# Kernel optimization log

Measured on AMD Instinct MI355X. Metric: run time of the kernel, lower is better.

The kernel has to match this reference:

```python
import jax, jax.numpy as jnp
import numpy as np

EPS = 1e-5
HEADS = 24
HEAD_DIM = 128


def _layernorm_noaffine(x):
    # LayerNorm over last dim (head_dim), elementwise_affine=False
    mu = jnp.mean(x, axis=-1, keepdims=True)
    var = jnp.mean(jnp.square(x - mu), axis=-1, keepdims=True)
    return (x - mu) / jnp.sqrt(var + EPS)


def _apply_rope(x, cos, sin):
    # diffusers apply_rotary_emb, use_real_unbind_dim=-2, sequence_dim=1
    # x: [B, S_img, H, D]; cos/sin: [S_img, D]
    x_real, x_imag = jnp.split(x, 2, axis=-1)               # halves of D
    x_rot = jnp.concatenate([-x_imag, x_real], axis=-1)
    return x * cos[None, :, None, :] + x_rot * sin[None, :, None, :]


def setup_inputs() -> dict:
    key = jax.random.key(0)
    ks = jax.random.split(key, 8)
    B, T, I, D = 2, 256, 1024, 3072
    inner = HEADS * HEAD_DIM
    return {
        "hidden_states": jax.random.normal(ks[0], (B, I, D), jnp.float32),
        "encoder_hidden_states": jax.random.normal(ks[1], (B, T, D), jnp.float32),
        "cos": jax.random.uniform(ks[2], (I, HEAD_DIM), jnp.float32),
        "sin": jax.random.uniform(ks[3], (I, HEAD_DIM), jnp.float32),
        "w_qkv": jax.random.normal(ks[4], (D, 3 * inner), jnp.float32) * 0.02,
        "b_qkv": jax.random.normal(ks[5], (3 * inner,), jnp.float32) * 0.02,
        "w_out": jax.random.normal(ks[6], (inner, D), jnp.float32) * 0.02,
        "b_out": jax.random.normal(ks[7], (D,), jnp.float32) * 0.02,
    }


def reference(hidden_states, encoder_hidden_states, cos, sin, w_qkv, b_qkv, w_out, b_out):
    text_len = encoder_hidden_states.shape[1]
    x = jnp.concatenate([encoder_hidden_states, hidden_states], axis=1)  # [B, S, D]
    B, S, _ = x.shape
    qkv = x @ w_qkv + b_qkv                                  # [B, S, 3*inner]
    q, k, v = jnp.split(qkv, 3, axis=-1)
    q = q.reshape(B, S, HEADS, HEAD_DIM)
    k = k.reshape(B, S, HEADS, HEAD_DIM)
    v = v.reshape(B, S, HEADS, HEAD_DIM)
    q = _layernorm_noaffine(q)
    k = _layernorm_noaffine(k)
    # partial RoPE: image tokens only
    q = jnp.concatenate([q[:, :text_len], _apply_rope(q[:, text_len:], cos, sin)], axis=1)
    k = jnp.concatenate([k[:, :text_len], _apply_rope(k[:, text_len:], cos, sin)], axis=1)
    # non-causal attention, scale = 1/sqrt(head_dim)
    scale = 1.0 / np.sqrt(HEAD_DIM).astype(np.float32)
    scores = jnp.einsum('bqhd,bkhd->bhqk', q, k) * scale
    attn = jax.nn.softmax(scores, axis=-1)
    out = jnp.einsum('bhqk,bkhd->bqhd', attn, v).reshape(B, S, HEADS * HEAD_DIM)
    out = out @ w_out + b_out                                # [B, S, D]
    return out[:, text_len:, :], out[:, :text_len, :]
```

## Files before the change

kernel.cpp:

```cpp
#include <hip/hip_runtime.h>

typedef unsigned short u16;
typedef __attribute__((ext_vector_type(8))) short bf16x8;
typedef __attribute__((ext_vector_type(4))) float f32x4;
typedef __attribute__((ext_vector_type(16))) float f32x16;

typedef const __attribute__((address_space(1))) void* gptr_t;
typedef __attribute__((address_space(3))) void* lptr_t;

__device__ __forceinline__ unsigned cvtpk_bf16(float a, float b){
  unsigned r; asm("v_cvt_pk_bf16_f32 %0, %1, %2" : "=v"(r) : "v"(a), "v"(b)); return r;
}
__device__ __forceinline__ u16 f2bf(float x){ return (u16)cvtpk_bf16(x, x); }
__device__ __forceinline__ float bf2f(u16 u){ union{unsigned i; float f;} v; v.i = ((unsigned)u)<<16; return v.f; }
__device__ __forceinline__ float fexp2(float x){ float r; asm("v_exp_f32 %0, %1" : "=v"(r) : "v"(x)); return r; }

__global__ __launch_bounds__(256) void prep_x_kernel(const float* __restrict__ hs,
                                                     const float* __restrict__ ehs,
                                                     u16* __restrict__ A){
  int idx = blockIdx.x*256 + threadIdx.x;
  int v = idx*4;
  int m = v/3072, c = v - m*3072;
  int b = m/1280, s = m - b*1280;
  const float* src = (s < 256) ? (ehs + ((size_t)(b*256+s))*3072 + c)
                               : (hs  + ((size_t)(b*1024+(s-256)))*3072 + c);
  float4 f = *(const float4*)src;
  uint2 o; o.x = cvtpk_bf16(f.x, f.y); o.y = cvtpk_bf16(f.z, f.w);
  *(uint2*)(A + v) = o;
}

__global__ __launch_bounds__(256) void transpose_w_kernel(const float* __restrict__ W,
                                                          u16* __restrict__ Wt,
                                                          int K, int N){
  __shared__ float t[64][36];
  int k0 = blockIdx.y*64, n0 = blockIdx.x*32;
  int tid = threadIdx.x;
  #pragma unroll
  for (int i=0;i<2;i++){
    int cell = i*256 + tid; int kl = cell>>3, nc = cell&7;
    *(float4*)&t[kl][nc*4] = *(const float4*)&W[(size_t)(k0+kl)*N + n0 + nc*4];
  }
  __syncthreads();
  #pragma unroll
  for (int i=0;i<2;i++){
    int chunk = i*256 + tid; int nl = chunk>>4, kc = chunk&15;
    float a = t[kc*4+0][nl], b2 = t[kc*4+1][nl], c2 = t[kc*4+2][nl], d2 = t[kc*4+3][nl];
    uint2 u; u.x = cvtpk_bf16(a, b2); u.y = cvtpk_bf16(c2, d2);
    *(uint2*)&Wt[(size_t)(n0+nl)*K + k0 + kc*4] = u;
  }
}

__global__ __launch_bounds__(512) void gemm256_kernel(const u16* __restrict__ A,
                                                      const u16* __restrict__ Bt,
                                                      const float* __restrict__ bias,
                                                      u16* __restrict__ C){
  const int K = 3072, N = 9216;
  __shared__ __align__(16) u16 lds[2][2][2][8192];
  int tid = threadIdx.x, wv = tid>>6, lane = tid&63;
  int wm = wv>>2, wn = wv&3;
  int l15 = lane&15, l4 = lane>>4;

  int bid = blockIdx.x;
  int wg = (bid&7)*45 + (bid>>3);
  int bm = wg/36, bn = wg%36;
  int m0 = bm*256, n0 = bn*256;

  int srow = tid>>2;
  int schn = (tid&3) ^ ((tid>>3)&3);
  const u16* aSrc = A  + (size_t)(m0 + srow)*K + schn*8;
  const u16* bSrc = Bt + (size_t)(n0 + srow)*K + schn*8;
  u16* ldsF = &lds[0][0][0][0];

  auto stagePair = [&](int Gp){
    int s = (Gp>>1)&1, h = Gp&1;
    size_t ko = (size_t)Gp*32;
    u16* la = ldsF + s*32768 + h*8192 + wv*512;
    u16* lb = la + 16384;
    const u16* a0 = aSrc + ko;
    const u16* b0 = bSrc + ko;
    __builtin_amdgcn_global_load_lds((gptr_t)a0,                 (lptr_t)la,        16,0,0);
    __builtin_amdgcn_global_load_lds((gptr_t)(a0+(size_t)128*K), (lptr_t)(la+4096), 16,0,0);
    __builtin_amdgcn_global_load_lds((gptr_t)b0,                 (lptr_t)lb,        16,0,0);
    __builtin_amdgcn_global_load_lds((gptr_t)(b0+(size_t)128*K), (lptr_t)(lb+4096), 16,0,0);
  };

  int fcs = l4 ^ ((l15>>1)&3);
  int aoff = (wm*128 + l15)*32 + fcs*8;
  int boff = (wn*64  + l15)*32 + fcs*8;

  f32x4 acc[8][4];
  #pragma unroll
  for (int r=0;r<8;r++)
    #pragma unroll
    for (int c=0;c<4;c++)
      #pragma unroll
      for (int q=0;q<4;q++) acc[r][c][q] = 0.f;

  stagePair(0); stagePair(1); stagePair(2);
  asm volatile("s_waitcnt vmcnt(8)" ::: "memory");
  __builtin_amdgcn_s_barrier();

  auto group = [&](int G, bool issue){
    const u16* rA = ldsF + ((G>>1)&1)*32768 + (G&1)*8192;
    const u16* rB = rA + 16384;
    bf16x8 af[8], bfv[4];
    #pragma unroll
    for (int r=0;r<8;r++) af[r] = *(const bf16x8*)(rA + aoff + r*512);
    #pragma unroll
    for (int c=0;c<4;c++) bfv[c] = *(const bf16x8*)(rB + boff + c*512);
    if (issue) stagePair(G+3);
    __builtin_amdgcn_s_setprio(1);
    #pragma unroll
    for (int r=0;r<8;r++)
      #pragma unroll
      for (int c=0;c<4;c++)
        acc[r][c] = __builtin_amdgcn_mfma_f32_16x16x32_bf16(af[r], bfv[c], acc[r][c], 0,0,0);
    __builtin_amdgcn_s_setprio(0);
  };

  for (int G=0; G<93; ++G){
    group(G, true);
    asm volatile("s_waitcnt vmcnt(8)" ::: "memory");
    __builtin_amdgcn_s_barrier();
  }
  group(93,false); asm volatile("s_waitcnt vmcnt(4)" ::: "memory"); __builtin_amdgcn_s_barrier();
  group(94,false); asm volatile("s_waitcnt vmcnt(0)" ::: "memory"); __builtin_amdgcn_s_barrier();
  group(95,false);

  #pragma unroll
  for (int r=0;r<8;r++){
    int row = m0 + wm*128 + r*16 + l4*4;
    #pragma unroll
    for (int c=0;c<4;c++){
      int col = n0 + wn*64 + c*16 + l15;
      float bv = bias[col];
      #pragma unroll
      for (int q=0;q<4;q++)
        C[(size_t)(row+q)*N + col] = f2bf(acc[r][c][q] + bv);
    }
  }
}

__global__ __launch_bounds__(256) void gemm_bt_kernel(const u16* __restrict__ A,
                                                      const u16* __restrict__ Bt,
                                                      const float* __restrict__ bias,
                                                      float* __restrict__ Cf,
                                                      int K, int N){
  __shared__ u16 As[2][4096];
  __shared__ u16 Bs[2][4096];
  int tid = threadIdx.x, wv = tid>>6, lane = tid&63;
  int l15 = lane & 15, l4 = lane >> 4;
  int m0 = blockIdx.y*128, n0 = blockIdx.x*128;
  int wr = wv>>1, wc = wv&1;

  f32x4 acc[4][4];
  #pragma unroll
  for (int i=0;i<4;i++)
    #pragma unroll
    for (int j=0;j<4;j++)
      #pragma unroll
      for (int r=0;r<4;r++) acc[i][j][r] = 0.f;

  const int NT = K >> 5;

  auto stage = [&](int buf, int kt){
    #pragma unroll
    for (int i=0;i<2;i++){
      int c = (wv*2+i)*64 + lane; int row = c>>2, kc = c&3;
      const u16* s = A + (size_t)(m0+row)*K + kt + kc*8;
      __builtin_amdgcn_global_load_lds((gptr_t)s, (lptr_t)(&As[buf][(wv*2+i)*512]), 16, 0, 0);
    }
    #pragma unroll
    for (int i=0;i<2;i++){
      int c = (wv*2+i)*64 + lane; int row = c>>2, kc = c&3;
      const u16* s = Bt + (size_t)(n0+row)*K + kt + kc*8;
      __builtin_amdgcn_global_load_lds((gptr_t)s, (lptr_t)(&Bs[buf][(wv*2+i)*512]), 16, 0, 0);
    }
  };

  stage(0, 0);
  __syncthreads();
  for (int t=0; t<NT; t++){
    int cur = t & 1;
    if (t+1 < NT) stage(cur^1, (t+1)*32);
    bf16x8 af[4], bfr[4];
    #pragma unroll
    for (int i=0;i<4;i++){
      af[i]  = *(const bf16x8*)&As[cur][(wr*64 + i*16 + l15)*32 + l4*8];
      bfr[i] = *(const bf16x8*)&Bs[cur][(wc*64 + i*16 + l15)*32 + l4*8];
    }
    #pragma unroll
    for (int i=0;i<4;i++)
      #pragma unroll
      for (int j=0;j<4;j++)
        acc[i][j] = __builtin_amdgcn_mfma_f32_16x16x32_bf16(af[i], bfr[j], acc[i][j], 0,0,0);
    __syncthreads();
  }

  #pragma unroll
  for (int i=0;i<4;i++){
    int row = m0 + wr*64 + i*16 + l4*4;
    #pragma unroll
    for (int j=0;j<4;j++){
      int col = n0 + wc*64 + j*16 + l15;
      float bv = bias[col];
      #pragma unroll
      for (int r=0;r<4;r++){
        int rr = row + r;
        int bb = rr / 1280; int s = rr - bb*1280;
        float* dst = (s < 256) ? (Cf + 6291456 + ((size_t)(bb*256 + s))*3072)
                               : (Cf + ((size_t)(bb*1024 + (s-256)))*3072);
        dst[col] = acc[i][j][r] + bv;
      }
    }
  }
}

__device__ __forceinline__ void ln_head(const u16* __restrict__ in, u16* __restrict__ out,
                                        const float* __restrict__ cosb, const float* __restrict__ sinb,
                                        int lane, int s, float scale){
  float x0 = bf2f(in[lane]), x1 = bf2f(in[64+lane]);
  float sum = x0 + x1;
  #pragma unroll
  for (int off=32; off>=1; off>>=1) sum += __shfl_xor(sum, off);
  float mean = sum * 0.0078125f;
  float d0 = x0-mean, d1 = x1-mean;
  float vs = d0*d0 + d1*d1;
  #pragma unroll
  for (int off=32; off>=1; off>>=1) vs += __shfl_xor(vs, off);
  float rstd = rsqrtf(vs*0.0078125f + 1e-5f);
  float y0 = d0*rstd, y1 = d1*rstd;
  if (s >= 256){
    int p = s - 256;
    float c0 = cosb[p*128 + lane], c1 = cosb[p*128 + 64 + lane];
    float s0 = sinb[p*128 + lane], s1 = sinb[p*128 + 64 + lane];
    float t0 = y0*c0 - y1*s0;
    float t1 = y1*c1 + y0*s1;
    y0 = t0; y1 = t1;
  }
  out[lane]    = f2bf(y0*scale);
  out[64+lane] = f2bf(y1*scale);
}

__global__ __launch_bounds__(256) void ln_rope_kernel(const u16* __restrict__ qkv,
                                                      const float* __restrict__ cosb,
                                                      const float* __restrict__ sinb,
                                                      u16* __restrict__ Q, u16* __restrict__ Kd){
  int g = blockIdx.x*4 + (threadIdx.x>>6);
  int lane = threadIdx.x & 63;
  int h = g % 24; int m = g / 24;
  int b = m / 1280; int s = m - b*1280;
  const u16* base = qkv + (size_t)m*9216 + h*128;
  size_t ho = ((size_t)(b*24 + h)*1280 + s)*128;
  ln_head(base,        Q  + ho, cosb, sinb, lane, s, 0.12751512f);
  ln_head(base + 3072, Kd + ho, cosb, sinb, lane, s, 1.0f);
}

__global__ __launch_bounds__(256) void v_transpose_kernel(const u16* __restrict__ qkv,
                                                          u16* __restrict__ Vt){
  __shared__ u16 tl[16384];
  int tid = threadIdx.x;
  int blk = blockIdx.x;
  int st = blk % 10; int bh = blk / 10; int b = bh/24, h = bh - b*24;
  #pragma unroll
  for (int i=0;i<8;i++){
    int idx = i*256 + tid; int s = idx>>4, dc = idx&15;
    int m = b*1280 + st*128 + s;
    bf16x8 v = *(const bf16x8*)(qkv + (size_t)m*9216 + 6144 + h*128 + dc*8);
    *(bf16x8*)(tl + (s*16 + (dc ^ ((s>>3)&7)))*8) = v;
  }
  __syncthreads();
  #pragma unroll
  for (int i=0;i<8;i++){
    int idx = i*256 + tid; int d = idx>>4, sc = idx&15;
    union { u16 t[8]; bf16x8 v; } tmp;
    #pragma unroll
    for (int j=0;j<8;j++){
      int s = sc*8 + j;
      tmp.t[j] = tl[(s*16 + ((d>>3) ^ ((s>>3)&7)))*8 + (d&7)];
    }
    *(bf16x8*)(Vt + ((size_t)bh*128 + d)*1280 + st*128 + sc*8) = tmp.v;
  }
}

__global__ __launch_bounds__(256) void attn_kernel(const u16* __restrict__ Q,
                                                   const u16* __restrict__ Kg,
                                                   const u16* __restrict__ Vt,
                                                   u16* __restrict__ AO){
  __shared__ __align__(16) u16 smem[32768];
  int tid = threadIdx.x, wv = tid>>6, lane = tid&63;
  int l31 = lane & 31, hi = lane >> 5;
  int blk = blockIdx.x;
  int qt = blk % 10; int bh = blk / 10;
  int b = bh / 24; int h = bh - b*24;
  const u16* Qb = Q  + (size_t)bh*1280*128;
  const u16* Kb = Kg + (size_t)bh*1280*128;
  const u16* Vb = Vt + (size_t)bh*128*1280;
  int q0 = qt*128 + wv*32;

  bf16x8 qf[8];
  #pragma unroll
  for (int ds=0; ds<8; ds++)
    qf[ds] = *(const bf16x8*)(Qb + (size_t)(q0 + l31)*128 + ds*16 + hi*8);

  f32x16 o[4];
  #pragma unroll
  for (int dc=0; dc<4; dc++)
    #pragma unroll
    for (int r=0;r<16;r++) o[dc][r] = 0.f;
  float mrun = -1e30f, lrun = 0.f;

  auto stage = [&](int t){
    int s0 = t*64; int bu = t&1;
    u16* Ksb = smem + bu*8192;
    u16* Vsb = smem + 16384 + bu*8192;
    #pragma unroll
    for (int i=0;i<4;i++){
      int c = (wv*4+i)*64 + lane; int key = c>>4, dc16 = c&15;
      const u16* src = Kb + (size_t)(s0+key)*128 + ((dc16 ^ (key&7))<<3);
      __builtin_amdgcn_global_load_lds((gptr_t)src, (lptr_t)(Ksb + (wv*4+i)*512), 16, 0, 0);
    }
    #pragma unroll
    for (int i=0;i<4;i++){
      int c = (wv*4+i)*64 + lane; int d = c>>3, kc = c&7;
      const u16* src = Vb + (size_t)d*1280 + s0 + ((kc ^ (d&7))<<3);
      __builtin_amdgcn_global_load_lds((gptr_t)src, (lptr_t)(Vsb + (wv*4+i)*512), 16, 0, 0);
    }
  };

  auto compute = [&](int t){
    const u16* Ks = smem + (t&1)*8192;
    const u16* Vs = smem + 16384 + (t&1)*8192;
    f32x16 sacc0, sacc1;
    #pragma unroll
    for (int r=0;r<16;r++){ sacc0[r]=0.f; sacc1[r]=0.f; }
    __builtin_amdgcn_s_setprio(1);
    #pragma unroll
    for (int ds=0; ds<8; ds++){
      int ch = ds*2 + hi;
      bf16x8 k0 = *(const bf16x8*)(Ks + (l31*16      + (ch ^ (l31 & 7)))*8);
      bf16x8 k1 = *(const bf16x8*)(Ks + ((32+l31)*16 + (ch ^ (l31 & 7)))*8);
      sacc0 = __builtin_amdgcn_mfma_f32_32x32x16_bf16(k0, qf[ds], sacc0, 0,0,0);
      sacc1 = __builtin_amdgcn_mfma_f32_32x32x16_bf16(k1, qf[ds], sacc1, 0,0,0);
    }
    __builtin_amdgcn_s_setprio(0);
    float mt = sacc0[0];
    #pragma unroll
    for (int r=1;r<16;r++) mt = fmaxf(mt, sacc0[r]);
    #pragma unroll
    for (int r=0;r<16;r++) mt = fmaxf(mt, sacc1[r]);
    mt = fmaxf(mt, __shfl_xor(mt, 32));
    float mnew = fmaxf(mrun, mt);
    float corr = fexp2(mrun - mnew);
    mrun = mnew;
    float p[32]; float ps = 0.f;
    #pragma unroll
    for (int r=0;r<16;r++){ p[r]    = fexp2(sacc0[r] - mnew); ps += p[r]; }
    #pragma unroll
    for (int r=0;r<16;r++){ p[16+r] = fexp2(sacc1[r] - mnew); ps += p[16+r]; }
    ps += __shfl_xor(ps, 32);
    lrun = lrun*corr + ps;
    #pragma unroll
    for (int dc=0; dc<4; dc++)
      #pragma unroll
      for (int r=0;r<16;r++) o[dc][r] *= corr;

    bf16x8 pf[4];
    #pragma unroll
    for (int c=0;c<4;c++){
      const float* pp = p + (c>>1)*16 + (c&1)*8;
      unsigned x0 = cvtpk_bf16(pp[0], pp[1]);
      unsigned y0 = cvtpk_bf16(pp[4], pp[5]);
      unsigned x1 = cvtpk_bf16(pp[2], pp[3]);
      unsigned y1 = cvtpk_bf16(pp[6], pp[7]);
      asm volatile("v_permlane32_swap_b32 %0, %1" : "+v"(x0), "+v"(y0));
      asm volatile("v_permlane32_swap_b32 %0, %1" : "+v"(x1), "+v"(y1));
      union { unsigned u[4]; bf16x8 v; } wb;
      wb.u[0]=x0; wb.u[1]=x1; wb.u[2]=y0; wb.u[3]=y1;
      pf[c] = wb.v;
    }
    __builtin_amdgcn_s_setprio(1);
    #pragma unroll
    for (int c=0;c<4;c++){
      #pragma unroll
      for (int dc=0;dc<4;dc++){
        int d = dc*32 + l31;
        bf16x8 vf = *(const bf16x8*)(Vs + (d*8 + ((2*c+hi) ^ (d&7)))*8);
        o[dc] = __builtin_amdgcn_mfma_f32_32x32x16_bf16(vf, pf[c], o[dc], 0,0,0);
      }
    }
    __builtin_amdgcn_s_setprio(0);
  };

  stage(0); stage(1);
  for (int t=0; t<19; ++t){
    asm volatile("s_waitcnt vmcnt(8)" ::: "memory");
    __builtin_amdgcn_s_barrier();
    compute(t);
    __builtin_amdgcn_s_barrier();
    if (t <= 17) stage(t+2);
  }
  asm volatile("s_waitcnt vmcnt(0)" ::: "memory");
  __builtin_amdgcn_s_barrier();
  compute(19);

  float rl = 1.f / lrun;
  __syncthreads();
  u16* ob = smem + wv*4096;
  #pragma unroll
  for (int dc=0; dc<4; dc++){
    #pragma unroll
    for (int rp=0; rp<8; rp++){
      int d = dc*32 + 2*(rp&1) + 8*(rp>>1) + 4*hi;
      unsigned u = cvtpk_bf16(o[dc][2*rp]*rl, o[dc][2*rp+1]*rl);
      int chs = (d>>3) ^ (l31 & 7);
      *(unsigned*)(ob + l31*128 + chs*8 + (d&7)) = u;
    }
  }
  __syncthreads();
  #pragma unroll
  for (int i=0;i<8;i++){
    int idx = i*64 + lane; int q = idx>>4, c8 = idx&15;
    bf16x8 vv = *(const bf16x8*)(ob + q*128 + ((c8 ^ (q&7))<<3));
    *(bf16x8*)(AO + (size_t)(b*1280 + q0 + q)*3072 + h*128 + c8*8) = vv;
  }
}

extern "C" void kernel_launch(void* const* d_in, const int* in_sizes, int n_in,
                              void* d_out, int out_size, void* d_ws, size_t ws_size,
                              hipStream_t stream){
  (void)in_sizes; (void)n_in; (void)out_size; (void)ws_size;
  const float* hs   = (const float*)d_in[0];
  const float* ehs  = (const float*)d_in[1];
  const float* cosb = (const float*)d_in[2];
  const float* sinb = (const float*)d_in[3];
  const float* wqkv = (const float*)d_in[4];
  const float* bqkv = (const float*)d_in[5];
  const float* wout = (const float*)d_in[6];
  const float* bout = (const float*)d_in[7];
  char* w = (char*)d_ws;
  size_t o = 0;
  u16* Abf = (u16*)(w + o); o += 15728640ull;
  u16* WqT = (u16*)(w + o); o += 56623104ull;
  u16* WoT = (u16*)(w + o); o += 18874368ull;
  u16* qkv = (u16*)(w + o); o += 47185920ull;
  u16* Qd  = (u16*)(w + o); o += 15728640ull;
  u16* Kd  = (u16*)(w + o); o += 15728640ull;
  u16* Vtd = (u16*)(w + o); o += 15728640ull;
  u16* AO  = (u16*)(w + o);
  float* out = (float*)d_out;

  prep_x_kernel<<<7680, 256, 0, stream>>>(hs, ehs, Abf);
  transpose_w_kernel<<<dim3(288,48), 256, 0, stream>>>(wqkv, WqT, 3072, 9216);
  transpose_w_kernel<<<dim3(96,48),  256, 0, stream>>>(wout, WoT, 3072, 3072);
  gemm256_kernel<<<360, 512, 0, stream>>>(Abf, WqT, bqkv, qkv);
  ln_rope_kernel<<<15360, 256, 0, stream>>>(qkv, cosb, sinb, Qd, Kd);
  v_transpose_kernel<<<480, 256, 0, stream>>>(qkv, Vtd);
  attn_kernel<<<480, 256, 0, stream>>>(Qd, Kd, Vtd, AO);
  gemm_bt_kernel<<<dim3(24,20), 256, 0, stream>>>(AO, WoT, bout, out, 3072, 3072);
}
```

Before: 572.0 us.

## Retile QKV GEMM to 256x192 with 4-stage LDS and add lazy softmax rescaling

```diff
diff --git a/kernel.cpp b/kernel.cpp
--- a/kernel.cpp
+++ b/kernel.cpp
@@ -14,6 +14,12 @@
 __device__ __forceinline__ u16 f2bf(float x){ return (u16)cvtpk_bf16(x, x); }
 __device__ __forceinline__ float bf2f(u16 u){ union{unsigned i; float f;} v; v.i = ((unsigned)u)<<16; return v.f; }
 __device__ __forceinline__ float fexp2(float x){ float r; asm("v_exp_f32 %0, %1" : "=v"(r) : "v"(x)); return r; }
+__device__ __forceinline__ float vmax16(f32x16 v){
+  float a0 = fmaxf(v[0],v[1]),  a1 = fmaxf(v[2],v[3]),  a2 = fmaxf(v[4],v[5]),  a3 = fmaxf(v[6],v[7]);
+  float a4 = fmaxf(v[8],v[9]),  a5 = fmaxf(v[10],v[11]),a6 = fmaxf(v[12],v[13]),a7 = fmaxf(v[14],v[15]);
+  float b0 = fmaxf(a0,a1), b1 = fmaxf(a2,a3), b2 = fmaxf(a4,a5), b3 = fmaxf(a6,a7);
+  return fmaxf(fmaxf(b0,b1), fmaxf(b2,b3));
+}
 
 __global__ __launch_bounds__(256) void prep_x_kernel(const float* __restrict__ hs,
                                                      const float* __restrict__ ehs,
@@ -50,80 +56,79 @@
   }
 }
 
-__global__ __launch_bounds__(512) void gemm256_kernel(const u16* __restrict__ A,
-                                                      const u16* __restrict__ Bt,
-                                                      const float* __restrict__ bias,
-                                                      u16* __restrict__ C){
+__global__ __launch_bounds__(512) void gemm_qkv_kernel(const u16* __restrict__ A,
+                                                       const u16* __restrict__ Bt,
+                                                       const float* __restrict__ bias,
+                                                       u16* __restrict__ C){
   const int K = 3072, N = 9216;
-  __shared__ __align__(16) u16 lds[2][2][2][8192];
+  __shared__ __align__(16) u16 lds[57344];
   int tid = threadIdx.x, wv = tid>>6, lane = tid&63;
   int wm = wv>>2, wn = wv&3;
   int l15 = lane&15, l4 = lane>>4;
 
   int bid = blockIdx.x;
-  int wg = (bid&7)*45 + (bid>>3);
-  int bm = wg/36, bn = wg%36;
-  int m0 = bm*256, n0 = bn*256;
-
-  int srow = tid>>2;
-  int schn = (tid&3) ^ ((tid>>3)&3);
-  const u16* aSrc = A  + (size_t)(m0 + srow)*K + schn*8;
-  const u16* bSrc = Bt + (size_t)(n0 + srow)*K + schn*8;
-  u16* ldsF = &lds[0][0][0][0];
-
-  auto stagePair = [&](int Gp){
-    int s = (Gp>>1)&1, h = Gp&1;
-    size_t ko = (size_t)Gp*32;
-    u16* la = ldsF + s*32768 + h*8192 + wv*512;
-    u16* lb = la + 16384;
-    const u16* a0 = aSrc + ko;
-    const u16* b0 = bSrc + ko;
-    __builtin_amdgcn_global_load_lds((gptr_t)a0,                 (lptr_t)la,        16,0,0);
-    __builtin_amdgcn_global_load_lds((gptr_t)(a0+(size_t)128*K), (lptr_t)(la+4096), 16,0,0);
-    __builtin_amdgcn_global_load_lds((gptr_t)b0,                 (lptr_t)lb,        16,0,0);
-    __builtin_amdgcn_global_load_lds((gptr_t)(b0+(size_t)128*K), (lptr_t)(lb+4096), 16,0,0);
+  int wg = (bid&7)*60 + (bid>>3);
+  int bm = wg/48, bn = wg%48;
+  int m0 = bm*256, n0 = bn*192;
+
+  int rlane = lane>>2;
+  int schn = (lane&3) ^ ((lane>>3)&3);
+  const u16* aS = A + (size_t)(m0 + wv*32 + rlane)*K + schn*8;
+  int brow = n0 + wv*32 + rlane; if (brow > 9215) brow = 9215;
+  const u16* bS = Bt + (size_t)brow*K + schn*8;
+
+  auto stagePair = [&](int G){
+    u16* base = lds + (G&3)*14336;
+    size_t ko = (size_t)G*32;
+    #pragma unroll
+    for (int j=0;j<2;j++)
+      __builtin_amdgcn_global_load_lds((gptr_t)(aS + (size_t)j*16*K + ko),
+                                       (lptr_t)(base + (wv*2+j)*512), 16,0,0);
+    if (wv < 6){
+      #pragma unroll
+      for (int j=0;j<2;j++)
+        __builtin_amdgcn_global_load_lds((gptr_t)(bS + (size_t)j*16*K + ko),
+                                         (lptr_t)(base + 8192 + (wv*2+j)*512), 16,0,0);
+    }
   };
 
   int fcs = l4 ^ ((l15>>1)&3);
-  int aoff = (wm*128 + l15)*32 + fcs*8;
-  int boff = (wn*64  + l15)*32 + fcs*8;
-
-  f32x4 acc[8][4];
+  f32x4 acc[8][3];
   #pragma unroll
   for (int r=0;r<8;r++)
     #pragma unroll
-    for (int c=0;c<4;c++)
+    for (int c=0;c<3;c++)
       #pragma unroll
       for (int q=0;q<4;q++) acc[r][c][q] = 0.f;
 
   stagePair(0); stagePair(1); stagePair(2);
-  asm volatile("s_waitcnt vmcnt(8)" ::: "memory");
+  asm volatile("s_waitcnt vmcnt(4)" ::: "memory");
   __builtin_amdgcn_s_barrier();
 
   auto group = [&](int G, bool issue){
-    const u16* rA = ldsF + ((G>>1)&1)*32768 + (G&1)*8192;
-    const u16* rB = rA + 16384;
-    bf16x8 af[8], bfv[4];
-    #pragma unroll
-    for (int r=0;r<8;r++) af[r] = *(const bf16x8*)(rA + aoff + r*512);
-    #pragma unroll
-    for (int c=0;c<4;c++) bfv[c] = *(const bf16x8*)(rB + boff + c*512);
+    const u16* rA = lds + (G&3)*14336;
+    const u16* rB = rA + 8192;
+    bf16x8 af[8], bfv[3];
+    #pragma unroll
+    for (int r=0;r<8;r++) af[r] = *(const bf16x8*)(rA + (wm*128 + r*16 + l15)*32 + fcs*8);
+    #pragma unroll
+    for (int c=0;c<3;c++) bfv[c] = *(const bf16x8*)(rB + (wn*48 + c*16 + l15)*32 + fcs*8);
     if (issue) stagePair(G+3);
     __builtin_amdgcn_s_setprio(1);
     #pragma unroll
     for (int r=0;r<8;r++)
       #pragma unroll
-      for (int c=0;c<4;c++)
+      for (int c=0;c<3;c++)
         acc[r][c] = __builtin_amdgcn_mfma_f32_16x16x32_bf16(af[r], bfv[c], acc[r][c], 0,0,0);
     __builtin_amdgcn_s_setprio(0);
   };
 
   for (int G=0; G<93; ++G){
     group(G, true);
-    asm volatile("s_waitcnt vmcnt(8)" ::: "memory");
+    asm volatile("s_waitcnt vmcnt(4)" ::: "memory");
     __builtin_amdgcn_s_barrier();
   }
-  group(93,false); asm volatile("s_waitcnt vmcnt(4)" ::: "memory"); __builtin_amdgcn_s_barrier();
+  group(93,false); asm volatile("s_waitcnt vmcnt(2)" ::: "memory"); __builtin_amdgcn_s_barrier();
   group(94,false); asm volatile("s_waitcnt vmcnt(0)" ::: "memory"); __builtin_amdgcn_s_barrier();
   group(95,false);
 
@@ -131,8 +136,8 @@
   for (int r=0;r<8;r++){
     int row = m0 + wm*128 + r*16 + l4*4;
     #pragma unroll
-    for (int c=0;c<4;c++){
-      int col = n0 + wn*64 + c*16 + l15;
+    for (int c=0;c<3;c++){
+      int col = n0 + wn*48 + c*16 + l15;
       float bv = bias[col];
       #pragma unroll
       for (int q=0;q<4;q++)
@@ -331,39 +336,54 @@
   auto compute = [&](int t){
     const u16* Ks = smem + (t&1)*8192;
     const u16* Vs = smem + 16384 + (t&1)*8192;
+    f32x16 sA, sB, sC, sD;
+    #pragma unroll
+    for (int r=0;r<16;r++){ sA[r]=0.f; sB[r]=0.f; sC[r]=0.f; sD[r]=0.f; }
+    __builtin_amdgcn_s_setprio(1);
+    #pragma unroll
+    for (int dp=0; dp<4; dp++){
+      int dsE = 2*dp, dsO = 2*dp+1;
+      int chE = dsE*2 + hi, chO = dsO*2 + hi;
+      bf16x8 k0E = *(const bf16x8*)(Ks + (l31*16      + (chE ^ (l31 & 7)))*8);
+      bf16x8 k1E = *(const bf16x8*)(Ks + ((32+l31)*16 + (chE ^ (l31 & 7)))*8);
+      bf16x8 k0O = *(const bf16x8*)(Ks + (l31*16      + (chO ^ (l31 & 7)))*8);
+      bf16x8 k1O = *(const bf16x8*)(Ks + ((32+l31)*16 + (chO ^ (l31 & 7)))*8);
+      sA = __builtin_amdgcn_mfma_f32_32x32x16_bf16(k0E, qf[dsE], sA, 0,0,0);
+      sC = __builtin_amdgcn_mfma_f32_32x32x16_bf16(k1E, qf[dsE], sC, 0,0,0);
+      sB = __builtin_amdgcn_mfma_f32_32x32x16_bf16(k0O, qf[dsO], sB, 0,0,0);
+      sD = __builtin_amdgcn_mfma_f32_32x32x16_bf16(k1O, qf[dsO], sD, 0,0,0);
+    }
+    __builtin_amdgcn_s_setprio(0);
     f32x16 sacc0, sacc1;
     #pragma unroll
-    for (int r=0;r<16;r++){ sacc0[r]=0.f; sacc1[r]=0.f; }
-    __builtin_amdgcn_s_setprio(1);
-    #pragma unroll
-    for (int ds=0; ds<8; ds++){
-      int ch = ds*2 + hi;
-      bf16x8 k0 = *(const bf16x8*)(Ks + (l31*16      + (ch ^ (l31 & 7)))*8);
-      bf16x8 k1 = *(const bf16x8*)(Ks + ((32+l31)*16 + (ch ^ (l31 & 7)))*8);
-      sacc0 = __builtin_amdgcn_mfma_f32_32x32x16_bf16(k0, qf[ds], sacc0, 0,0,0);
-      sacc1 = __builtin_amdgcn_mfma_f32_32x32x16_bf16(k1, qf[ds], sacc1, 0,0,0);
-    }
-    __builtin_amdgcn_s_setprio(0);
-    float mt = sacc0[0];
-    #pragma unroll
-    for (int r=1;r<16;r++) mt = fmaxf(mt, sacc0[r]);
-    #pragma unroll
-    for (int r=0;r<16;r++) mt = fmaxf(mt, sacc1[r]);
+    for (int r=0;r<16;r++){ sacc0[r] = sA[r]+sB[r]; sacc1[r] = sC[r]+sD[r]; }
+
+    float mt = fmaxf(vmax16(sacc0), vmax16(sacc1));
     mt = fmaxf(mt, __shfl_xor(mt, 32));
-    float mnew = fmaxf(mrun, mt);
-    float corr = fexp2(mrun - mnew);
+    int noresc = __all(mt <= mrun + 11.5f);
+    float mnew, corr;
+    if (noresc){ mnew = mrun; corr = 1.f; }
+    else       { mnew = fmaxf(mrun, mt); corr = fexp2(mrun - mnew); }
     mrun = mnew;
-    float p[32]; float ps = 0.f;
-    #pragma unroll
-    for (int r=0;r<16;r++){ p[r]    = fexp2(sacc0[r] - mnew); ps += p[r]; }
-    #pragma unroll
-    for (int r=0;r<16;r++){ p[16+r] = fexp2(sacc1[r] - mnew); ps += p[16+r]; }
+    float p[32];
+    float ps0=0.f, ps1=0.f, ps2=0.f, ps3=0.f;
+    #pragma unroll
+    for (int r=0;r<8;r++){ p[r]    = fexp2(sacc0[r]   - mnew); ps0 += p[r]; }
+    #pragma unroll
+    for (int r=0;r<8;r++){ p[8+r]  = fexp2(sacc0[8+r] - mnew); ps1 += p[8+r]; }
+    #pragma unroll
+    for (int r=0;r<8;r++){ p[16+r] = fexp2(sacc1[r]   - mnew); ps2 += p[16+r]; }
+    #pragma unroll
+    for (int r=0;r<8;r++){ p[24+r] = fexp2(sacc1[8+r] - mnew); ps3 += p[24+r]; }
+    float ps = (ps0+ps1) + (ps2+ps3);
     ps += __shfl_xor(ps, 32);
     lrun = lrun*corr + ps;
-    #pragma unroll
-    for (int dc=0; dc<4; dc++)
-      #pragma unroll
-      for (int r=0;r<16;r++) o[dc][r] *= corr;
+    if (!noresc){
+      #pragma unroll
+      for (int dc=0; dc<4; dc++)
+        #pragma unroll
+        for (int r=0;r<16;r++) o[dc][r] *= corr;
+    }
 
     bf16x8 pf[4];
     #pragma unroll
@@ -453,7 +473,7 @@
   prep_x_kernel<<<7680, 256, 0, stream>>>(hs, ehs, Abf);
   transpose_w_kernel<<<dim3(288,48), 256, 0, stream>>>(wqkv, WqT, 3072, 9216);
   transpose_w_kernel<<<dim3(96,48),  256, 0, stream>>>(wout, WoT, 3072, 3072);
-  gemm256_kernel<<<360, 512, 0, stream>>>(Abf, WqT, bqkv, qkv);
+  gemm_qkv_kernel<<<480, 512, 0, stream>>>(Abf, WqT, bqkv, qkv);
   ln_rope_kernel<<<15360, 256, 0, stream>>>(qkv, cosb, sinb, Qd, Kd);
   v_transpose_kernel<<<480, 256, 0, stream>>>(qkv, Vtd);
   attn_kernel<<<480, 256, 0, stream>>>(Qd, Kd, Vtd, AO);
```

Measured after the change: 558.2 us. 1.02x faster.
